# Performance work log

Measured on AMD Instinct MI355X. Metric: run time of the kernel, lower is better.

Reference implementation:

```python
import jax, jax.numpy as jnp
import numpy as np

B, N, M, C = 4, 2048, 576, 512
H, KVH, D = 8, 2, 64          # heads, kv heads, head_dim
E, TOPK, F = 8, 2, 2048       # experts, top-k, expert hidden (4*C)
EPS = 1e-6
NEG = -1e9


def setup_inputs() -> dict:
    key = jax.random.key(0)
    ks = iter(jax.random.split(key, 40))
    w = lambda shape, s=0.02: jax.random.normal(next(ks), shape, jnp.float32) * s
    d = {
        'x': jax.random.normal(next(ks), (B, N, C), jnp.float32),
        'vision_features': jax.random.normal(next(ks), (B, M, C), jnp.float32),
        'ln1_g': jnp.ones((C,), jnp.float32), 'ln1_b': jnp.zeros((C,), jnp.float32),
        'ln2_g': jnp.ones((C,), jnp.float32), 'ln2_b': jnp.zeros((C,), jnp.float32),
        'ln3_g': jnp.ones((C,), jnp.float32), 'ln3_b': jnp.zeros((C,), jnp.float32),
        # self-attention (GQA): q -> C, k/v -> KVH*D
        'sa_wq': w((C, C)), 'sa_bq': jnp.zeros((C,), jnp.float32),
        'sa_wk': w((C, KVH * D)), 'sa_bk': jnp.zeros((KVH * D,), jnp.float32),
        'sa_wv': w((C, KVH * D)), 'sa_bv': jnp.zeros((KVH * D,), jnp.float32),
        'sa_wo': w((C, C)), 'sa_bo': jnp.zeros((C,), jnp.float32),
        # cross-attention (GQA)
        'ca_wq': w((C, C)), 'ca_bq': jnp.zeros((C,), jnp.float32),
        'ca_wk': w((C, KVH * D)), 'ca_bk': jnp.zeros((KVH * D,), jnp.float32),
        'ca_wv': w((C, KVH * D)), 'ca_bv': jnp.zeros((KVH * D,), jnp.float32),
        'ca_wo': w((C, C)), 'ca_bo': jnp.zeros((C,), jnp.float32),
        # MoE: router + stacked expert MLPs (C -> F -> C, GELU)
        'router_w': w((C, E)), 'router_b': jnp.zeros((E,), jnp.float32),
        'e_w1': w((E, C, F)), 'e_b1': jnp.zeros((E, F), jnp.float32),
        'e_w2': w((E, F, C)), 'e_b2': jnp.zeros((E, C), jnp.float32),
    }
    return d


def _ln(x, g, b):
    mu = jnp.mean(x, -1, keepdims=True)
    var = jnp.mean(jnp.square(x - mu), -1, keepdims=True)
    return (x - mu) * jax.lax.rsqrt(var + EPS) * g + b


def _gqa_attn(xq, ctx, wq, bq, wk, bk, wv, bv, wo, bo, causal):
    b, n, c = xq.shape
    m = ctx.shape[1]
    q = (xq @ wq + bq).reshape(b, n, H, D).transpose(0, 2, 1, 3)      # bhnd
    k = (ctx @ wk + bk).reshape(b, m, KVH, D).transpose(0, 2, 1, 3)   # bgmd
    v = (ctx @ wv + bv).reshape(b, m, KVH, D).transpose(0, 2, 1, 3)
    rep = H // KVH
    k = jnp.repeat(k, rep, axis=1)  # repeat_interleave over head dim
    v = jnp.repeat(v, rep, axis=1)
    scores = jnp.einsum('bhnd,bhmd->bhnm', q, k) * (D ** -0.5)
    if causal:
        mask = jnp.tril(jnp.ones((n, m), bool))
        scores = jnp.where(mask, scores, NEG)
    a = jax.nn.softmax(scores, axis=-1)
    o = jnp.einsum('bhnm,bhmd->bhnd', a, v).transpose(0, 2, 1, 3).reshape(b, n, c)
    return o @ wo + bo


def _moe(x, router_w, router_b, e_w1, e_b1, e_w2, e_b2):
    logits = x @ router_w + router_b                    # [B,N,E]
    probs = jax.nn.softmax(logits, axis=-1)
    topv, topi = jax.lax.top_k(probs, TOPK)             # [B,N,K]
    topv = topv / jnp.sum(topv, -1, keepdims=True)      # renormalize top-k gates
    onehot = jax.nn.one_hot(topi, E, dtype=x.dtype)     # [B,N,K,E]
    gates = jnp.einsum('bnke,bnk->bne', onehot, topv)   # sparse gates, zeros off top-k
    h = jax.nn.gelu(jnp.einsum('bnc,ecf->bnef', x, e_w1) + e_b1)
    eo = jnp.einsum('bnef,efc->bnec', h, e_w2) + e_b2
    out = jnp.einsum('bne,bnec->bnc', gates, eo)
    # load-balance aux loss (Switch-style): E * sum_e f_e * P_e
    dispatch = jnp.sum(onehot, axis=2)                  # [B,N,E] routed mask
    f = jnp.mean(dispatch, axis=(0, 1))
    P = jnp.mean(probs, axis=(0, 1))
    aux = E * jnp.sum(f * P)
    return out, aux


def reference(x, vision_features,
              ln1_g, ln1_b, ln2_g, ln2_b, ln3_g, ln3_b,
              sa_wq, sa_bq, sa_wk, sa_bk, sa_wv, sa_bv, sa_wo, sa_bo,
              ca_wq, ca_bq, ca_wk, ca_bk, ca_wv, ca_bv, ca_wo, ca_bo,
              router_w, router_b, e_w1, e_b1, e_w2, e_b2):
    # pre-norm causal self-attn + residual
    h = _ln(x, ln1_g, ln1_b)
    x = x + _gqa_attn(h, h, sa_wq, sa_bq, sa_wk, sa_bk, sa_wv, sa_bv, sa_wo, sa_bo, True)
    # pre-norm cross-attn + residual
    h = _ln(x, ln2_g, ln2_b)
    x = x + _gqa_attn(h, vision_features, ca_wq, ca_bq, ca_wk, ca_bk, ca_wv, ca_bv, ca_wo, ca_bo, False)
    # pre-norm MoE FFN + residual
    h = _ln(x, ln3_g, ln3_b)
    m, aux = _moe(h, router_w, router_b, e_w1, e_b1, e_w2, e_b2)
    return x + m, aux
```

## Files before the change

kernel.cpp:

```cpp
#include <hip/hip_runtime.h>
#include <cstddef>
#include <cstdint>

#define B_   4
#define N_   2048
#define M_   576
#define C_   512
#define H_   8
#define KVH_ 2
#define D_   64
#define E_   8
#define F_   2048
#define BN_  (B_*N_)
#define BM_  (B_*M_)

typedef __attribute__((ext_vector_type(8))) short bf16x8;
typedef __attribute__((ext_vector_type(4))) float f32x4;

__device__ __forceinline__ unsigned short f2bf(float f) {
    union { float f; unsigned int u; } v; v.f = f;
    unsigned int r = v.u + 0x7FFFu + ((v.u >> 16) & 1u);
    return (unsigned short)(r >> 16);
}
__device__ __forceinline__ float bf2f(unsigned short u) {
    union { unsigned int u; float f; } v; v.u = ((unsigned int)u) << 16;
    return v.f;
}

typedef __attribute__((address_space(1))) void glb_void;
typedef __attribute__((address_space(3))) void lds_void;
__device__ __forceinline__ void gl2lds16(const unsigned short* g, unsigned short* l) {
    __builtin_amdgcn_global_load_lds((glb_void*)g, (lds_void*)l, 16, 0, 0);
}

__global__ __launch_bounds__(256) void prep_all(
    const float* __restrict__ sa_wq, const float* __restrict__ sa_wk,
    const float* __restrict__ sa_wv, const float* __restrict__ sa_wo,
    const float* __restrict__ ca_wq, const float* __restrict__ ca_wk,
    const float* __restrict__ ca_wv, const float* __restrict__ ca_wo,
    const float* __restrict__ e_w1, const float* __restrict__ e_w2,
    const float* __restrict__ vis,
    const float* __restrict__ sa_bk, const float* __restrict__ sa_bv,
    const float* __restrict__ ca_bk, const float* __restrict__ ca_bv,
    unsigned short* __restrict__ sa_wqt, unsigned short* __restrict__ sa_wkvt,
    unsigned short* __restrict__ sa_wot,
    unsigned short* __restrict__ ca_wqt, unsigned short* __restrict__ ca_wkvt,
    unsigned short* __restrict__ ca_wot,
    unsigned short* __restrict__ w1t, unsigned short* __restrict__ w2t,
    unsigned short* __restrict__ visbf,
    float* __restrict__ bkv_sa, float* __restrict__ bkv_ca,
    int* __restrict__ ctrl)
{
    __shared__ float T[32][33];
    int t = blockIdx.x;
    int tid = threadIdx.x;

    if (t < 17664) {
        const float* W; unsigned short* Wt; int K, N, kt, nt;
        if (t < 1280) {
            if (t < 256)      { W = sa_wq; Wt = sa_wqt; K = 512; N = 512; int r = t;        nt = r & 15; kt = r >> 4; }
            else if (t < 320) { W = sa_wk; Wt = sa_wkvt;            K = 512; N = 128; int r = t - 256; nt = r & 3;  kt = r >> 2; }
            else if (t < 384) { W = sa_wv; Wt = sa_wkvt + 128*512;  K = 512; N = 128; int r = t - 320; nt = r & 3;  kt = r >> 2; }
            else if (t < 640) { W = sa_wo; Wt = sa_wot; K = 512; N = 512; int r = t - 384;  nt = r & 15; kt = r >> 4; }
            else if (t < 896) { W = ca_wq; Wt = ca_wqt; K = 512; N = 512; int r = t - 640;  nt = r & 15; kt = r >> 4; }
            else if (t < 960) { W = ca_wk; Wt = ca_wkvt;            K = 512; N = 128; int r = t - 896; nt = r & 3;  kt = r >> 2; }
            else if (t < 1024){ W = ca_wv; Wt = ca_wkvt + 128*512;  K = 512; N = 128; int r = t - 960; nt = r & 3;  kt = r >> 2; }
            else              { W = ca_wo; Wt = ca_wot; K = 512; N = 512; int r = t - 1024; nt = r & 15; kt = r >> 4; }
        } else if (t < 9472) {
            int r = t - 1280; int e = r >> 10; r &= 1023;
            W = e_w1 + (size_t)e * C_ * F_; Wt = w1t + (size_t)e * C_ * F_;
            K = C_; N = F_; nt = r & 63; kt = r >> 6;
        } else {
            int r = t - 9472; int e = r >> 10; r &= 1023;
            W = e_w2 + (size_t)e * F_ * C_; Wt = w2t + (size_t)e * F_ * C_;
            K = F_; N = C_; nt = r & 15; kt = r >> 4;
        }
        int rr = tid >> 3, c4 = (tid & 7) * 4;
        int k0 = kt * 32, n0 = nt * 32;
        float4 v = *(const float4*)&W[(size_t)(k0 + rr) * N + n0 + c4];
        T[rr][c4 + 0] = v.x; T[rr][c4 + 1] = v.y; T[rr][c4 + 2] = v.z; T[rr][c4 + 3] = v.w;
        __syncthreads();
        ushort4 o;
        o.x = f2bf(T[c4 + 0][rr]); o.y = f2bf(T[c4 + 1][rr]);
        o.z = f2bf(T[c4 + 2][rr]); o.w = f2bf(T[c4 + 3][rr]);
        *(ushort4*)&Wt[(size_t)(n0 + rr) * K + k0 + c4] = o;
    } else if (t < 18816) {
        int i = (t - 17664) * 1024 + tid * 4;
        float4 v = *(const float4*)(vis + i);
        ushort4 o;
        o.x = f2bf(v.x); o.y = f2bf(v.y); o.z = f2bf(v.z); o.w = f2bf(v.w);
        *(ushort4*)(visbf + i) = o;
    } else {
        if (tid < 128) {
            bkv_sa[tid]       = sa_bk[tid];
            bkv_sa[128 + tid] = sa_bv[tid];
            bkv_ca[tid]       = ca_bk[tid];
            bkv_ca[128 + tid] = ca_bv[tid];
        }
        if (tid < 32) ctrl[tid] = 0;
    }
}

__global__ __launch_bounds__(256) void ln_bf(const float* __restrict__ x,
    const float* __restrict__ g, const float* __restrict__ b, unsigned short* __restrict__ out)
{
    int row = blockIdx.x;
    const float* xr = x + (size_t)row * C_;
    float s = 0.f, ss = 0.f;
    for (int c = threadIdx.x; c < C_; c += 256) { float v = xr[c]; s += v; ss += v * v; }
    __shared__ float S1[256], S2[256];
    S1[threadIdx.x] = s; S2[threadIdx.x] = ss;
    __syncthreads();
    for (int o = 128; o > 0; o >>= 1) {
        if (threadIdx.x < o) { S1[threadIdx.x] += S1[threadIdx.x + o]; S2[threadIdx.x] += S2[threadIdx.x + o]; }
        __syncthreads();
    }
    float mu  = S1[0] * (1.f / C_);
    float var = S2[0] * (1.f / C_) - mu * mu;
    float inv = rsqrtf(var + 1e-6f);
    unsigned short* orow = out + (size_t)row * C_;
    for (int c = threadIdx.x; c < C_; c += 256)
        orow[c] = f2bf((xr[c] - mu) * inv * g[c] + b[c]);
}

__global__ __launch_bounds__(256) void ln_dual(const float* __restrict__ x,
    const float* __restrict__ g, const float* __restrict__ b,
    float* __restrict__ outF, unsigned short* __restrict__ outBf)
{
    int row = blockIdx.x;
    const float* xr = x + (size_t)row * C_;
    float s = 0.f, ss = 0.f;
    for (int c = threadIdx.x; c < C_; c += 256) { float v = xr[c]; s += v; ss += v * v; }
    __shared__ float S1[256], S2[256];
    S1[threadIdx.x] = s; S2[threadIdx.x] = ss;
    __syncthreads();
    for (int o = 128; o > 0; o >>= 1) {
        if (threadIdx.x < o) { S1[threadIdx.x] += S1[threadIdx.x + o]; S2[threadIdx.x] += S2[threadIdx.x + o]; }
        __syncthreads();
    }
    float mu  = S1[0] * (1.f / C_);
    float var = S2[0] * (1.f / C_) - mu * mu;
    float inv = rsqrtf(var + 1e-6f);
    for (int c = threadIdx.x; c < C_; c += 256) {
        float v = (xr[c] - mu) * inv * g[c] + b[c];
        outF[(size_t)row * C_ + c] = v;
        outBf[(size_t)row * C_ + c] = f2bf(v);
    }
}

__global__ __launch_bounds__(256) void dense_mfma(
    const unsigned short* __restrict__ Abf,
    const unsigned short* __restrict__ Btbf,
    const float* __restrict__ bias,
    const float* __restrict__ xin,
    float* __restrict__ outF,
    unsigned short* __restrict__ outBf,
    unsigned short* __restrict__ outBf2,
    int N, int K, int mode, int NkPer)
{
    int row0 = blockIdx.y * 128;
    int col0 = blockIdx.x * 128;

    __shared__ unsigned short As[128 * 32];
    __shared__ unsigned short Bs[128 * 32];

    int tid = threadIdx.x;
    int lane = tid & 63, wid = tid >> 6;
    int lrow = lane >> 2;
    int cswz = (((lane & 3) ^ ((lane >> 3) & 3)) << 3);
    int ar0 = 16 * (wid * 2) + lrow;
    int ar1 = ar0 + 16;
    const unsigned short* gA0 = Abf + (size_t)(row0 + ar0) * K + cswz;
    const unsigned short* gA1 = Abf + (size_t)(row0 + ar1) * K + cswz;
    const unsigned short* gB0 = Btbf + (size_t)(col0 + ar0) * K + cswz;
    const unsigned short* gB1 = Btbf + (size_t)(col0 + ar1) * K + cswz;
    unsigned short* lA0 = As + (wid * 2) * 512;
    unsigned short* lA1 = lA0 + 512;
    unsigned short* lB0 = Bs + (wid * 2) * 512;
    unsigned short* lB1 = lB0 + 512;

    int wm0 = (wid & 1) * 64, wn0 = (wid >> 1) * 64;
    int lm = lane & 15, lq = lane >> 4;
    int swb = (lq ^ ((lm >> 1) & 3)) << 3;
    int aoff[4], boff[4];
#pragma unroll
    for (int i = 0; i < 4; i++) {
        aoff[i] = (wm0 + 16 * i + lm) * 32 + swb;
        boff[i] = (wn0 + 16 * i + lm) * 32 + swb;
    }

    f32x4 acc[4][4];
#pragma unroll
    for (int i = 0; i < 4; i++)
#pragma unroll
        for (int j = 0; j < 4; j++)
            acc[i][j] = (f32x4){0.f, 0.f, 0.f, 0.f};

    for (int k0 = 0; k0 < K; k0 += 32) {
        __syncthreads();
        gl2lds16(gA0 + k0, lA0);
        gl2lds16(gA1 + k0, lA1);
        gl2lds16(gB0 + k0, lB0);
        gl2lds16(gB1 + k0, lB1);
        __syncthreads();

        bf16x8 av[4], bv[4];
#pragma unroll
        for (int i = 0; i < 4; i++) av[i] = *(const bf16x8*)&As[aoff[i]];
#pragma unroll
        for (int i = 0; i < 4; i++) bv[i] = *(const bf16x8*)&Bs[boff[i]];
#pragma unroll
        for (int mi = 0; mi < 4; mi++)
#pragma unroll
            for (int ni = 0; ni < 4; ni++)
                acc[mi][ni] = __builtin_amdgcn_mfma_f32_16x16x32_bf16(av[mi], bv[ni], acc[mi][ni], 0, 0, 0);
    }

#pragma unroll
    for (int mi = 0; mi < 4; mi++) {
#pragma unroll
        for (int ri = 0; ri < 4; ri++) {
            int gr = row0 + wm0 + 16 * mi + lq * 4 + ri;
            if (mode == 3) {
#pragma unroll
                for (int ni = 0; ni < 4; ni++) {
                    int gc = col0 + wn0 + 16 * ni + lm;
                    float v = acc[mi][ni][ri] + bias[gc];
                    if (gc < 128) {
                        outBf[(size_t)gr * 128 + gc] = f2bf(v);
                    } else {
                        int bb = gr / NkPer;
                        int mm = gr - bb * NkPer;
                        outBf2[((size_t)bb * 128 + (gc - 128)) * NkPer + mm] = f2bf(v);
                    }
                }
            } else if (mode == 1) {
                size_t orow = (size_t)gr * N;
#pragma unroll
                for (int ni = 0; ni < 4; ni++) {
                    int gc = col0 + wn0 + 16 * ni + lm;
                    outF[orow + gc] += acc[mi][ni][ri] + bias[gc];
                }
            } else if (mode == 4) {
                size_t orow = (size_t)gr * N;
#pragma unroll
                for (int ni = 0; ni < 4; ni++) {
                    int gc = col0 + wn0 + 16 * ni + lm;
                    outF[orow + gc] = xin[orow + gc] + acc[mi][ni][ri] + bias[gc];
                }
            } else {
                size_t orow = (size_t)gr * N;
#pragma unroll
                for (int ni = 0; ni < 4; ni++) {
                    int gc = col0 + wn0 + 16 * ni + lm;
                    outBf[orow + gc] = f2bf(acc[mi][ni][ri] + bias[gc]);
                }
            }
        }
    }
}

__global__ __launch_bounds__(256) void attn_mfma(
    const unsigned short* __restrict__ Q,
    const unsigned short* __restrict__ K,
    const unsigned short* __restrict__ Vt,
    unsigned short* __restrict__ Obf,
    float* __restrict__ Opart,
    float* __restrict__ Lpart,
    int NkPer, int causal)
{
    __shared__ unsigned short Qs[64 * 72];
    __shared__ unsigned short Ks[64 * 72];
    __shared__ unsigned short Vs[64 * 72];
    unsigned short* Ps = Qs;

    int tid = threadIdx.x;
    int qt = blockIdx.x, bh = blockIdx.y, z = blockIdx.z;
    int b = bh >> 3, h = bh & 7, g = h >> 2;
    int q0 = qt * 64;

#pragma unroll
    for (int i = 0; i < 2; i++) {
        int s = tid + (i << 8);
        int r = s >> 3, c8 = (s & 7) << 3;
        *(uint4*)&Qs[r * 72 + c8] =
            *(const uint4*)&Q[(size_t)(b * N_ + q0 + r) * C_ + h * D_ + c8];
    }
    __syncthreads();

    int lane = tid & 63, wid = tid >> 6;
    int lm = lane & 15, lq = lane >> 4;
    int arow = wid * 16 + lm;

    bf16x8 qf[2];
    qf[0] = *(const bf16x8*)&Qs[arow * 72 + lq * 8];
    qf[1] = *(const bf16x8*)&Qs[arow * 72 + lq * 8 + 32];

    float lsum[4];
    f32x4 of[4];
#pragma unroll
    for (int i = 0; i < 4; i++) { lsum[i] = 0.f; of[i] = (f32x4){0.f,0.f,0.f,0.f}; }

    int nkt = causal ? (qt + 1) : ((NkPer + 63) >> 6);
    int nz = gridDim.z;
    int per = (nkt + nz - 1) / nz;
    int kt0 = z * per;
    int kt1 = min(nkt, kt0 + per);

    for (int kt = kt0; kt < kt1; kt++) {
        int k0 = kt << 6;
        __syncthreads();
#pragma unroll
        for (int i = 0; i < 2; i++) {
            int s = tid + (i << 8);
            int r = s >> 3, c8 = (s & 7) << 3;
            *(uint4*)&Ks[r * 72 + c8] =
                *(const uint4*)&K[(size_t)(b * NkPer + k0 + r) * (KVH_ * D_) + g * D_ + c8];
            *(uint4*)&Vs[r * 72 + c8] =
                *(const uint4*)&Vt[(size_t)(b * (KVH_ * D_) + g * D_ + r) * NkPer + k0 + c8];
        }
        __syncthreads();

        f32x4 sf[4];
#pragma unroll
        for (int i = 0; i < 4; i++) sf[i] = (f32x4){0.f,0.f,0.f,0.f};
#pragma unroll
        for (int ks = 0; ks < 2; ks++) {
#pragma unroll
            for (int ni = 0; ni < 4; ni++) {
                bf16x8 bv = *(const bf16x8*)&Ks[(16 * ni + lm) * 72 + lq * 8 + 32 * ks];
                sf[ni] = __builtin_amdgcn_mfma_f32_16x16x32_bf16(qf[ks], bv, sf[ni], 0, 0, 0);
            }
        }

        bool diag = causal && (k0 + 63 > q0 + wid * 16);
#pragma unroll
        for (int ni = 0; ni < 4; ni++)
#pragma unroll
            for (int ri = 0; ri < 4; ri++) {
                float v = sf[ni][ri] * 0.125f - 8.f;
                if (diag && (k0 + 16 * ni + lm > q0 + wid * 16 + lq * 4 + ri)) v = -1e30f;
                float p = __expf(v);
                sf[ni][ri] = p;
                lsum[ri] += p;
            }

#pragma unroll
        for (int ni = 0; ni < 4; ni++)
#pragma unroll
            for (int ri = 0; ri < 4; ri++)
                Ps[(wid * 16 + lq * 4 + ri) * 72 + 16 * ni + lm] = f2bf(sf[ni][ri]);
        __syncthreads();

        bf16x8 pf0 = *(const bf16x8*)&Ps[arow * 72 + lq * 8];
        bf16x8 pf1 = *(const bf16x8*)&Ps[arow * 72 + lq * 8 + 32];
#pragma unroll
        for (int ni = 0; ni < 4; ni++) {
            bf16x8 vv0 = *(const bf16x8*)&Vs[(16 * ni + lm) * 72 + lq * 8];
            bf16x8 vv1 = *(const bf16x8*)&Vs[(16 * ni + lm) * 72 + lq * 8 + 32];
            of[ni] = __builtin_amdgcn_mfma_f32_16x16x32_bf16(pf0, vv0, of[ni], 0, 0, 0);
            of[ni] = __builtin_amdgcn_mfma_f32_16x16x32_bf16(pf1, vv1, of[ni], 0, 0, 0);
        }
    }

#pragma unroll
    for (int ri = 0; ri < 4; ri++) {
        float s = lsum[ri];
        s += __shfl_xor(s, 1);
        s += __shfl_xor(s, 2);
        s += __shfl_xor(s, 4);
        s += __shfl_xor(s, 8);
        lsum[ri] = s;
    }

    if (nz == 1) {
#pragma unroll
        for (int ri = 0; ri < 4; ri++) {
            float inv = 1.f / lsum[ri];
            int q = q0 + wid * 16 + lq * 4 + ri;
            size_t orow = (size_t)(b * N_ + q) * C_ + h * D_;
#pragma unroll
            for (int ni = 0; ni < 4; ni++)
                Obf[orow + 16 * ni + lm] = f2bf(of[ni][ri] * inv);
        }
    } else {
        size_t zofs = (size_t)z * BN_ * C_;
#pragma unroll
        for (int ri = 0; ri < 4; ri++) {
            int q = q0 + wid * 16 + lq * 4 + ri;
            size_t orow = zofs + (size_t)(b * N_ + q) * C_ + h * D_;
#pragma unroll
            for (int ni = 0; ni < 4; ni++)
                Opart[orow + 16 * ni + lm] = of[ni][ri];
            if (lm == 0)
                Lpart[(size_t)z * (B_ * H_ * N_) + bh * N_ + q] = lsum[ri];
        }
    }
}

__global__ __launch_bounds__(256) void attn_combine(const float* __restrict__ Opart,
    const float* __restrict__ Lpart, unsigned short* __restrict__ Obf)
{
    int flat = (blockIdx.x * 256 + threadIdx.x) * 4;
    int row = flat >> 9, col = flat & 511;
    int b = row >> 11, q = row & (N_ - 1), h = col >> 6;
    int bh = b * 8 + h;
    float l = Lpart[bh * N_ + q] + Lpart[B_ * H_ * N_ + bh * N_ + q];
    float inv = 1.f / l;
    float4 o0 = *(const float4*)&Opart[flat];
    float4 o1 = *(const float4*)&Opart[(size_t)BN_ * C_ + flat];
    ushort4 o;
    o.x = f2bf((o0.x + o1.x) * inv); o.y = f2bf((o0.y + o1.y) * inv);
    o.z = f2bf((o0.z + o1.z) * inv); o.w = f2bf((o0.w + o1.w) * inv);
    *(ushort4*)&Obf[flat] = o;
}

__global__ __launch_bounds__(256) void router_logits(const float* __restrict__ X,
    const float* __restrict__ RW, const float* __restrict__ RB,
    float* __restrict__ gprobs, int* __restrict__ topi, float* __restrict__ gatesv)
{
    int lane = threadIdx.x & 63;
    int t = blockIdx.x * 4 + (threadIdx.x >> 6);
    const float* xr = X + (size_t)t * C_;
    float p[8] = {};
    for (int i = 0; i < 8; i++) {
        int c = i * 64 + lane;
        float xv = xr[c];
#pragma unroll
        for (int e = 0; e < 8; e++) p[e] = fmaf(xv, RW[c * 8 + e], p[e]);
    }
#pragma unroll
    for (int e = 0; e < 8; e++) {
        float v = p[e];
        v += __shfl_xor(v, 32, 64);
        v += __shfl_xor(v, 16, 64);
        v += __shfl_xor(v, 8, 64);
        v += __shfl_xor(v, 4, 64);
        v += __shfl_xor(v, 2, 64);
        v += __shfl_xor(v, 1, 64);
        p[e] = v;
    }
    if (lane == 0) {
        float logits[8], mx = -1e30f;
        for (int e = 0; e < 8; e++) { logits[e] = p[e] + RB[e]; mx = fmaxf(mx, logits[e]); }
        float pr[8], sum = 0.f;
        for (int e = 0; e < 8; e++) { pr[e] = expf(logits[e] - mx); sum += pr[e]; }
        float inv = 1.f / sum;
        for (int e = 0; e < 8; e++) { pr[e] *= inv; gprobs[t * 8 + e] = pr[e]; }
        int i1 = 0;
        for (int e = 1; e < 8; e++) if (pr[e] > pr[i1]) i1 = e;
        int i2 = (i1 == 0) ? 1 : 0;
        for (int e = 0; e < 8; e++) if (e != i1 && pr[e] > pr[i2]) i2 = e;
        float v1 = pr[i1], v2 = pr[i2], sg = 1.f / (v1 + v2);
        topi[t * 2]     = i1;  topi[t * 2 + 1]   = i2;
        gatesv[t * 2]   = v1 * sg;  gatesv[t * 2 + 1] = v2 * sg;
    }
}

__global__ __launch_bounds__(256) void router_reduce(const float* __restrict__ gprobs,
    const int* __restrict__ topi, int* __restrict__ ctrl, float* __restrict__ psum)
{
    __shared__ float fs[256];
    __shared__ int   is_[256];
    int bid = blockIdx.x, tid = threadIdx.x;
    if (bid < 8) {
        float s = 0.f;
        for (int t = tid; t < BN_; t += 256) s += gprobs[t * 8 + bid];
        fs[tid] = s; __syncthreads();
        for (int o = 128; o > 0; o >>= 1) { if (tid < o) fs[tid] += fs[tid + o]; __syncthreads(); }
        if (tid == 0) psum[bid] = fs[0];
    } else {
        int e = bid - 8, c = 0;
        for (int i = tid; i < BN_ * 2; i += 256) c += (topi[i] == e);
        is_[tid] = c; __syncthreads();
        for (int o = 128; o > 0; o >>= 1) { if (tid < o) is_[tid] += is_[tid + o]; __syncthreads(); }
        if (tid == 0) ctrl[e] = is_[0];
    }
}

__global__ void router_offsets(int* __restrict__ ctrl)
{
    if (threadIdx.x == 0 && blockIdx.x == 0) {
        int off = 0;
        for (int e = 0; e < 8; e++) {
            ctrl[16 + e] = off;
            off += (ctrl[e] + 127) & ~127;
        }
        ctrl[24] = off;
    }
}

__global__ __launch_bounds__(256) void router_scatter(const int* __restrict__ topi,
    const float* __restrict__ gatesv, int* __restrict__ rowtok,
    int* __restrict__ slotidx, int* __restrict__ ctrl)
{
    __shared__ int lcnt[8];
    __shared__ int lbase[8];
    int tid = threadIdx.x;
    int t = blockIdx.x * 256 + tid;
    if (tid < 8) lcnt[tid] = 0;
    __syncthreads();
    int e0 = topi[t * 2], e1 = topi[t * 2 + 1];
    int p0 = atomicAdd(&lcnt[e0], 1);
    int p1 = atomicAdd(&lcnt[e1], 1);
    __syncthreads();
    if (tid < 8) lbase[tid] = atomicAdd(&ctrl[8 + tid], lcnt[tid]);
    __syncthreads();
    int s0 = ctrl[16 + e0] + lbase[e0] + p0;
    int s1 = ctrl[16 + e1] + lbase[e1] + p1;
    rowtok[s0] = t;
    rowtok[s1] = t;
    slotidx[t * 2]     = s0;
    slotidx[t * 2 + 1] = s1;
}

__global__ __launch_bounds__(256) void moe_mfma(
    const unsigned short* __restrict__ Abf,
    const unsigned short* __restrict__ Btbf,
    const float* __restrict__ biasAll,
    unsigned short* __restrict__ outBf,
    const int* __restrict__ rowtok,
    const int* __restrict__ ctrl,
    int N, int K, int mode)
{
    int e = blockIdx.z;
    int cnt = ctrl[e];
    int row0 = blockIdx.x * 128;
    if (row0 >= cnt) return;
    int off = ctrl[16 + e];
    int col0 = blockIdx.y * 128;
    const unsigned short* Bt = Btbf + (size_t)e * N * K;
    const float* bias = biasAll + (size_t)e * N;

    __shared__ unsigned short As[128 * 32];
    __shared__ unsigned short Bs[128 * 32];
    __shared__ __align__(16) unsigned short Cs[4][32 * 72];
    __shared__ int toks[128];

    int tid = threadIdx.x;
    if (mode == 1 && tid < 128) {
        int gl = row0 + tid;
        toks[tid] = rowtok[off + (gl < cnt ? gl : 0)];
    }
    __syncthreads();

    int lane = tid & 63, wid = tid >> 6;
    int lrow = lane >> 2;
    int cswz = (((lane & 3) ^ ((lane >> 3) & 3)) << 3);
    int ar0 = 16 * (wid * 2) + lrow;
    int ar1 = ar0 + 16;
    const unsigned short *gA0, *gA1;
    if (mode == 1) {
        gA0 = Abf + (size_t)toks[ar0] * K + cswz;
        gA1 = Abf + (size_t)toks[ar1] * K + cswz;
    } else {
        gA0 = Abf + (size_t)(off + row0 + ar0) * K + cswz;
        gA1 = Abf + (size_t)(off + row0 + ar1) * K + cswz;
    }
    const unsigned short* gB0 = Bt + (size_t)(col0 + ar0) * K + cswz;
    const unsigned short* gB1 = Bt + (size_t)(col0 + ar1) * K + cswz;
    unsigned short* lA0 = As + (wid * 2) * 512;
    unsigned short* lA1 = lA0 + 512;
    unsigned short* lB0 = Bs + (wid * 2) * 512;
    unsigned short* lB1 = lB0 + 512;

    int wm0 = (wid & 1) * 64, wn0 = (wid >> 1) * 64;
    int lm = lane & 15, lq = lane >> 4;
    int swb = (lq ^ ((lm >> 1) & 3)) << 3;
    int aoff[4], boff[4];
#pragma unroll
    for (int i = 0; i < 4; i++) {
        aoff[i] = (wm0 + 16 * i + lm) * 32 + swb;
        boff[i] = (wn0 + 16 * i + lm) * 32 + swb;
    }

    f32x4 acc[4][4];
#pragma unroll
    for (int i = 0; i < 4; i++)
#pragma unroll
        for (int j = 0; j < 4; j++)
            acc[i][j] = (f32x4){0.f, 0.f, 0.f, 0.f};

    for (int k0 = 0; k0 < K; k0 += 32) {
        __syncthreads();
        gl2lds16(gA0 + k0, lA0);
        gl2lds16(gA1 + k0, lA1);
        gl2lds16(gB0 + k0, lB0);
        gl2lds16(gB1 + k0, lB1);
        __syncthreads();

        bf16x8 av[4], bv[4];
#pragma unroll
        for (int i = 0; i < 4; i++) av[i] = *(const bf16x8*)&As[aoff[i]];
#pragma unroll
        for (int i = 0; i < 4; i++) bv[i] = *(const bf16x8*)&Bs[boff[i]];
#pragma unroll
        for (int mi = 0; mi < 4; mi++)
#pragma unroll
            for (int ni = 0; ni < 4; ni++)
                acc[mi][ni] = __builtin_amdgcn_mfma_f32_16x16x32_bf16(av[mi], bv[ni], acc[mi][ni], 0, 0, 0);
    }

    unsigned short* cs = Cs[wid];
#pragma unroll
    for (int p = 0; p < 2; p++) {
#pragma unroll
        for (int m2 = 0; m2 < 2; m2++) {
            int mi = 2 * p + m2;
#pragma unroll
            for (int ri = 0; ri < 4; ri++) {
                int gl = row0 + wm0 + 16 * mi + lq * 4 + ri;
                bool valid = gl < cnt;
#pragma unroll
                for (int ni = 0; ni < 4; ni++) {
                    int gc = col0 + wn0 + 16 * ni + lm;
                    float xv = acc[mi][ni][ri] + bias[gc];
                    float hv;
                    if (mode == 1) {
                        float z = 0.7978845608f * xv * fmaf(0.044715f, xv * xv, 1.f);
                        hv = valid ? __fdividef(xv, 1.f + __expf(-2.f * z)) : 0.f;
                    } else {
                        hv = xv;
                    }
                    cs[(m2 * 16 + lq * 4 + ri) * 72 + 16 * ni + lm] = f2bf(hv);
                }
            }
        }
        int rr = lane >> 1;
        int ch = (lane & 1) * 32;
        int gl2 = row0 + wm0 + 32 * p + rr;
        size_t orow = (size_t)(off + gl2) * N + col0 + wn0 + ch;
        const unsigned short* rsrc = &cs[rr * 72 + ch];
#pragma unroll
        for (int j = 0; j < 4; j++)
            *(uint4*)&outBf[orow + j * 8] = *(const uint4*)&rsrc[j * 8];
    }
}

__global__ __launch_bounds__(256) void moe_combine(const unsigned short* __restrict__ slots,
    const int* __restrict__ slotidx, const float* __restrict__ gatesv,
    float* __restrict__ out)
{
    int flat = (blockIdx.x * 256 + threadIdx.x) * 4;
    int t = flat >> 9, c = flat & 511;
    int s0 = slotidx[t * 2], s1 = slotidx[t * 2 + 1];
    float g0 = gatesv[t * 2], g1 = gatesv[t * 2 + 1];
    ushort4 a = *(const ushort4*)&slots[(size_t)s0 * C_ + c];
    ushort4 b = *(const ushort4*)&slots[(size_t)s1 * C_ + c];
    float4 o = *(float4*)&out[flat];
    o.x += g0 * bf2f(a.x) + g1 * bf2f(b.x);
    o.y += g0 * bf2f(a.y) + g1 * bf2f(b.y);
    o.z += g0 * bf2f(a.z) + g1 * bf2f(b.z);
    o.w += g0 * bf2f(a.w) + g1 * bf2f(b.w);
    *(float4*)&out[flat] = o;
}

__global__ void aux_kernel(const int* __restrict__ ctrl, const float* __restrict__ psum,
                           float* __restrict__ outaux)
{
    if (threadIdx.x == 0 && blockIdx.x == 0) {
        float s = 0.f;
        for (int e = 0; e < 8; e++)
            s += ((float)ctrl[e] / (float)BN_) * (psum[e] / (float)BN_);
        outaux[0] = 8.f * s;
    }
}

extern "C" void kernel_launch(void* const* d_in, const int* in_sizes, int n_in,
                              void* d_out, int out_size, void* d_ws, size_t ws_size,
                              hipStream_t stream)
{
    const float* x      = (const float*)d_in[0];
    const float* vis    = (const float*)d_in[1];
    const float* ln1g   = (const float*)d_in[2];
    const float* ln1b   = (const float*)d_in[3];
    const float* ln2g   = (const float*)d_in[4];
    const float* ln2b   = (const float*)d_in[5];
    const float* ln3g   = (const float*)d_in[6];
    const float* ln3b   = (const float*)d_in[7];
    const float* sa_wq  = (const float*)d_in[8];
    const float* sa_bq  = (const float*)d_in[9];
    const float* sa_wk  = (const float*)d_in[10];
    const float* sa_bk  = (const float*)d_in[11];
    const float* sa_wv  = (const float*)d_in[12];
    const float* sa_bv  = (const float*)d_in[13];
    const float* sa_wo  = (const float*)d_in[14];
    const float* sa_bo  = (const float*)d_in[15];
    const float* ca_wq  = (const float*)d_in[16];
    const float* ca_bq  = (const float*)d_in[17];
    const float* ca_wk  = (const float*)d_in[18];
    const float* ca_bk  = (const float*)d_in[19];
    const float* ca_wv  = (const float*)d_in[20];
    const float* ca_bv  = (const float*)d_in[21];
    const float* ca_wo  = (const float*)d_in[22];
    const float* ca_bo  = (const float*)d_in[23];
    const float* rw     = (const float*)d_in[24];
    const float* rb     = (const float*)d_in[25];
    const float* e_w1   = (const float*)d_in[26];
    const float* e_b1   = (const float*)d_in[27];
    const float* e_w2   = (const float*)d_in[28];
    const float* e_b2   = (const float*)d_in[29];

    float* out = (float*)d_out;

    char* ws = (char*)d_ws;
    size_t off = 0;
    auto alloc = [&](size_t bytes) -> void* {
        void* p = ws + off;
        off = (off + bytes + 255) & ~(size_t)255;
        return p;
    };
    float* hbuf    = (float*)alloc((size_t)BN_ * C_ * 4);
    unsigned short* hbz = (unsigned short*)alloc((size_t)BN_ * C_ * 2);
    unsigned short* visbf = (unsigned short*)alloc((size_t)BM_ * C_ * 2);
    unsigned short* eoslots = (unsigned short*)hbuf;
    char* ureg = (char*)alloc((size_t)17408 * F_ * 2);
    unsigned short* moeH = (unsigned short*)ureg;
    unsigned short* qbf  = (unsigned short*)(ureg);
    unsigned short* obf  = (unsigned short*)(ureg + (size_t)BN_ * C_ * 2);
    unsigned short* kbf  = (unsigned short*)(ureg + (size_t)BN_ * C_ * 4);
    unsigned short* vtbf = (unsigned short*)(ureg + (size_t)BN_ * C_ * 4 + (size_t)BN_ * KVH_ * D_ * 2);
    float* opart = (float*)(ureg + (size_t)BN_ * C_ * 4 + (size_t)BN_ * KVH_ * D_ * 4);
    float* lpart = (float*)(ureg + (size_t)BN_ * C_ * 4 + (size_t)BN_ * KVH_ * D_ * 4
                                 + (size_t)2 * BN_ * C_ * 4);
    unsigned short* sa_wqt = (unsigned short*)alloc((size_t)C_ * C_ * 2);
    unsigned short* sa_wkvt = (unsigned short*)alloc((size_t)C_ * 2 * KVH_ * D_ * 2);
    unsigned short* sa_wot = (unsigned short*)alloc((size_t)C_ * C_ * 2);
    unsigned short* ca_wqt = (unsigned short*)alloc((size_t)C_ * C_ * 2);
    unsigned short* ca_wkvt = (unsigned short*)alloc((size_t)C_ * 2 * KVH_ * D_ * 2);
    unsigned short* ca_wot = (unsigned short*)alloc((size_t)C_ * C_ * 2);
    float* bkv_sa = (float*)alloc(256 * 4);
    float* bkv_ca = (float*)alloc(256 * 4);
    unsigned short* w1t  = (unsigned short*)alloc((size_t)E_ * C_ * F_ * 2);
    unsigned short* w2t  = (unsigned short*)alloc((size_t)E_ * F_ * C_ * 2);
    float* gprobs  = (float*)alloc((size_t)BN_ * 8 * 4);
    int*   topi    = (int*)  alloc((size_t)BN_ * 2 * 4);
    float* gatesv  = (float*)alloc((size_t)BN_ * 2 * 4);
    int*   rowtok  = (int*)  alloc(17408 * 4);
    int*   slotidx = (int*)  alloc((size_t)BN_ * 2 * 4);
    int*   ctrl    = (int*)  alloc(256);
    float* psum    = (float*)((char*)ctrl + 128);
    (void)ws_size; (void)in_sizes; (void)n_in; (void)out_size;

    prep_all<<<18817, 256, 0, stream>>>(
        sa_wq, sa_wk, sa_wv, sa_wo, ca_wq, ca_wk, ca_wv, ca_wo,
        e_w1, e_w2, vis, sa_bk, sa_bv, ca_bk, ca_bv,
        sa_wqt, sa_wkvt, sa_wot, ca_wqt, ca_wkvt, ca_wot,
        w1t, w2t, visbf, bkv_sa, bkv_ca, ctrl);

    ln_bf<<<BN_, 256, 0, stream>>>(x, ln1g, ln1b, hbz);
    dense_mfma<<<dim3(4, 64), 256, 0, stream>>>(hbz, sa_wqt, sa_bq, nullptr, nullptr, qbf, nullptr, C_, C_, 0, 0);
    dense_mfma<<<dim3(2, 64), 256, 0, stream>>>(hbz, sa_wkvt, bkv_sa, nullptr, nullptr, kbf, vtbf, 256, C_, 3, N_);
    attn_mfma<<<dim3(N_/64, B_*H_, 2), 256, 0, stream>>>(qbf, kbf, vtbf, nullptr, opart, lpart, N_, 1);
    attn_combine<<<(BN_*C_)/1024, 256, 0, stream>>>(opart, lpart, obf);
    dense_mfma<<<dim3(4, 64), 256, 0, stream>>>(obf, sa_wot, sa_bo, x, out, nullptr, nullptr, C_, C_, 4, 0);

    ln_bf<<<BN_, 256, 0, stream>>>(out, ln2g, ln2b, hbz);
    dense_mfma<<<dim3(4, 64), 256, 0, stream>>>(hbz, ca_wqt, ca_bq, nullptr, nullptr, qbf, nullptr, C_, C_, 0, 0);
    dense_mfma<<<dim3(2, 18), 256, 0, stream>>>(visbf, ca_wkvt, bkv_ca, nullptr, nullptr, kbf, vtbf, 256, C_, 3, M_);
    attn_mfma<<<dim3(N_/64, B_*H_, 1), 256, 0, stream>>>(qbf, kbf, vtbf, obf, nullptr, nullptr, M_, 0);
    dense_mfma<<<dim3(4, 64), 256, 0, stream>>>(obf, ca_wot, ca_bo, nullptr, out, nullptr, nullptr, C_, C_, 1, 0);

    ln_dual<<<BN_, 256, 0, stream>>>(out, ln3g, ln3b, hbuf, hbz);
    router_logits<<<BN_/4, 256, 0, stream>>>(hbuf, rw, rb, gprobs, topi, gatesv);
    router_reduce<<<16, 256, 0, stream>>>(gprobs, topi, ctrl, psum);
    router_offsets<<<1, 1, 0, stream>>>(ctrl);
    router_scatter<<<BN_/256, 256, 0, stream>>>(topi, gatesv, rowtok, slotidx, ctrl);
    moe_mfma<<<dim3(BN_/128, F_/128, E_), 256, 0, stream>>>(
        hbz, w1t, e_b1, moeH, rowtok, ctrl, F_, C_, 1);
    moe_mfma<<<dim3(BN_/128, C_/128, E_), 256, 0, stream>>>(
        moeH, w2t, e_b2, eoslots, rowtok, ctrl, C_, F_, 2);
    moe_combine<<<(BN_*C_)/1024, 256, 0, stream>>>(eoslots, slotidx, gatesv, out);
    aux_kernel<<<1, 1, 0, stream>>>(ctrl, psum, out + (size_t)BN_ * C_);
}
```

Baseline: 729.7 us.

## Deepen MoE GEMM K-tile to 64 with XOR swizzle and direct epilogue stores

The MoE expert GEMM kernel now stages 64-wide K slices per iteration with an 8-way XOR swizzle, halving the number of barrier pairs per tile. The grid is transposed so column tiles vary fastest, letting consecutive blocks share the same A rows in cache. The LDS-staged coalesced epilogue is replaced by direct scalar bf16 stores from accumulators, which frees LDS but produces narrower, less coalesced global writes.

```diff
diff --git a/kernel.cpp b/kernel.cpp
--- a/kernel.cpp
+++ b/kernel.cpp
@@ -525,16 +525,15 @@
 {
     int e = blockIdx.z;
     int cnt = ctrl[e];
-    int row0 = blockIdx.x * 128;
+    int row0 = blockIdx.y * 128;
     if (row0 >= cnt) return;
     int off = ctrl[16 + e];
-    int col0 = blockIdx.y * 128;
+    int col0 = blockIdx.x * 128;
     const unsigned short* Bt = Btbf + (size_t)e * N * K;
     const float* bias = biasAll + (size_t)e * N;
 
-    __shared__ unsigned short As[128 * 32];
-    __shared__ unsigned short Bs[128 * 32];
-    __shared__ __align__(16) unsigned short Cs[4][32 * 72];
+    __shared__ unsigned short As[128 * 64];
+    __shared__ unsigned short Bs[128 * 64];
     __shared__ int toks[128];
 
     int tid = threadIdx.x;
@@ -545,33 +544,33 @@
     __syncthreads();
 
     int lane = tid & 63, wid = tid >> 6;
-    int lrow = lane >> 2;
-    int cswz = (((lane & 3) ^ ((lane >> 3) & 3)) << 3);
-    int ar0 = 16 * (wid * 2) + lrow;
-    int ar1 = ar0 + 16;
-    const unsigned short *gA0, *gA1;
-    if (mode == 1) {
-        gA0 = Abf + (size_t)toks[ar0] * K + cswz;
-        gA1 = Abf + (size_t)toks[ar1] * K + cswz;
-    } else {
-        gA0 = Abf + (size_t)(off + row0 + ar0) * K + cswz;
-        gA1 = Abf + (size_t)(off + row0 + ar1) * K + cswz;
-    }
-    const unsigned short* gB0 = Bt + (size_t)(col0 + ar0) * K + cswz;
-    const unsigned short* gB1 = Bt + (size_t)(col0 + ar1) * K + cswz;
-    unsigned short* lA0 = As + (wid * 2) * 512;
-    unsigned short* lA1 = lA0 + 512;
-    unsigned short* lB0 = Bs + (wid * 2) * 512;
-    unsigned short* lB1 = lB0 + 512;
+    int r8 = lane >> 3;
+    size_t asrc[4], bsrc[4];
+    unsigned short *adst[4], *bdst[4];
+#pragma unroll
+    for (int i = 0; i < 4; i++) {
+        int rA = wid * 32 + i * 8 + r8;
+        int srcc = (((lane & 7) ^ (rA & 7)) << 3);
+        size_t arow = (mode == 1) ? (size_t)toks[rA] * K
+                                  : (size_t)(off + row0 + rA) * K;
+        asrc[i] = arow + srcc;
+        bsrc[i] = (size_t)(col0 + rA) * K + srcc;
+        adst[i] = As + (wid * 32 + i * 8) * 64;
+        bdst[i] = Bs + (wid * 32 + i * 8) * 64;
+    }
 
     int wm0 = (wid & 1) * 64, wn0 = (wid >> 1) * 64;
     int lm = lane & 15, lq = lane >> 4;
-    int swb = (lq ^ ((lm >> 1) & 3)) << 3;
-    int aoff[4], boff[4];
+    int x7 = lm & 7;
+    int aoff[4][2], boff[4][2];
 #pragma unroll
     for (int i = 0; i < 4; i++) {
-        aoff[i] = (wm0 + 16 * i + lm) * 32 + swb;
-        boff[i] = (wn0 + 16 * i + lm) * 32 + swb;
+#pragma unroll
+        for (int ks = 0; ks < 2; ks++) {
+            int swz = (((ks << 2) + lq) ^ x7) << 3;
+            aoff[i][ks] = (wm0 + 16 * i + lm) * 64 + swz;
+            boff[i][ks] = (wn0 + 16 * i + lm) * 64 + swz;
+        }
     }
 
     f32x4 acc[4][4];
@@ -581,59 +580,56 @@
         for (int j = 0; j < 4; j++)
             acc[i][j] = (f32x4){0.f, 0.f, 0.f, 0.f};
 
-    for (int k0 = 0; k0 < K; k0 += 32) {
-        __syncthreads();
-        gl2lds16(gA0 + k0, lA0);
-        gl2lds16(gA1 + k0, lA1);
-        gl2lds16(gB0 + k0, lB0);
-        gl2lds16(gB1 + k0, lB1);
-        __syncthreads();
-
-        bf16x8 av[4], bv[4];
-#pragma unroll
-        for (int i = 0; i < 4; i++) av[i] = *(const bf16x8*)&As[aoff[i]];
-#pragma unroll
-        for (int i = 0; i < 4; i++) bv[i] = *(const bf16x8*)&Bs[boff[i]];
-#pragma unroll
-        for (int mi = 0; mi < 4; mi++)
-#pragma unroll
-            for (int ni = 0; ni < 4; ni++)
-                acc[mi][ni] = __builtin_amdgcn_mfma_f32_16x16x32_bf16(av[mi], bv[ni], acc[mi][ni], 0, 0, 0);
-    }
-
-    unsigned short* cs = Cs[wid];
-#pragma unroll
-    for (int p = 0; p < 2; p++) {
-#pragma unroll
-        for (int m2 = 0; m2 < 2; m2++) {
-            int mi = 2 * p + m2;
-#pragma unroll
-            for (int ri = 0; ri < 4; ri++) {
-                int gl = row0 + wm0 + 16 * mi + lq * 4 + ri;
-                bool valid = gl < cnt;
+    for (int k0 = 0; k0 < K; k0 += 64) {
+        __syncthreads();
+#pragma unroll
+        for (int i = 0; i < 4; i++) {
+            gl2lds16(Abf + asrc[i] + k0, adst[i]);
+            gl2lds16(Bt  + bsrc[i] + k0, bdst[i]);
+        }
+        __syncthreads();
+
+#pragma unroll
+        for (int ks = 0; ks < 2; ks++) {
+            bf16x8 av[4], bv[4];
+#pragma unroll
+            for (int i = 0; i < 4; i++) av[i] = *(const bf16x8*)&As[aoff[i][ks]];
+#pragma unroll
+            for (int i = 0; i < 4; i++) bv[i] = *(const bf16x8*)&Bs[boff[i][ks]];
+#pragma unroll
+            for (int mi = 0; mi < 4; mi++)
+#pragma unroll
+                for (int ni = 0; ni < 4; ni++)
+                    acc[mi][ni] = __builtin_amdgcn_mfma_f32_16x16x32_bf16(av[mi], bv[ni], acc[mi][ni], 0, 0, 0);
+        }
+    }
+
+#pragma unroll
+    for (int mi = 0; mi < 4; mi++) {
+#pragma unroll
+        for (int ri = 0; ri < 4; ri++) {
+            int gl = row0 + wm0 + 16 * mi + lq * 4 + ri;
+            size_t orow = (size_t)(off + gl) * N;
+            if (mode == 1) {
 #pragma unroll
                 for (int ni = 0; ni < 4; ni++) {
                     int gc = col0 + wn0 + 16 * ni + lm;
-                    float xv = acc[mi][ni][ri] + bias[gc];
-                    float hv;
-                    if (mode == 1) {
+                    float hv = 0.f;
+                    if (gl < cnt) {
+                        float xv = acc[mi][ni][ri] + bias[gc];
                         float z = 0.7978845608f * xv * fmaf(0.044715f, xv * xv, 1.f);
-                        hv = valid ? __fdividef(xv, 1.f + __expf(-2.f * z)) : 0.f;
-                    } else {
-                        hv = xv;
+                        hv = __fdividef(xv, 1.f + __expf(-2.f * z));
                     }
-                    cs[(m2 * 16 + lq * 4 + ri) * 72 + 16 * ni + lm] = f2bf(hv);
+                    outBf[orow + gc] = f2bf(hv);
+                }
+            } else {
+#pragma unroll
+                for (int ni = 0; ni < 4; ni++) {
+                    int gc = col0 + wn0 + 16 * ni + lm;
+                    outBf[orow + gc] = f2bf(acc[mi][ni][ri] + bias[gc]);
                 }
             }
         }
-        int rr = lane >> 1;
-        int ch = (lane & 1) * 32;
-        int gl2 = row0 + wm0 + 32 * p + rr;
-        size_t orow = (size_t)(off + gl2) * N + col0 + wn0 + ch;
-        const unsigned short* rsrc = &cs[rr * 72 + ch];
-#pragma unroll
-        for (int j = 0; j < 4; j++)
-            *(uint4*)&outBf[orow + j * 8] = *(const uint4*)&rsrc[j * 8];
     }
 }
 
@@ -766,9 +762,9 @@
     router_reduce<<<16, 256, 0, stream>>>(gprobs, topi, ctrl, psum);
     router_offsets<<<1, 1, 0, stream>>>(ctrl);
     router_scatter<<<BN_/256, 256, 0, stream>>>(topi, gatesv, rowtok, slotidx, ctrl);
-    moe_mfma<<<dim3(BN_/128, F_/128, E_), 256, 0, stream>>>(
+    moe_mfma<<<dim3(F_/128, BN_/128, E_), 256, 0, stream>>>(
         hbz, w1t, e_b1, moeH, rowtok, ctrl, F_, C_, 1);
-    moe_mfma<<<dim3(BN_/128, C_/128, E_), 256, 0, stream>>>(
+    moe_mfma<<<dim3(C_/128, BN_/128, E_), 256, 0, stream>>>(
         moeH, w2t, e_b2, eoslots, rowtok, ctrl, C_, F_, 2);
     moe_combine<<<(BN_*C_)/1024, 256, 0, stream>>>(eoslots, slotidx, gatesv, out);
     aux_kernel<<<1, 1, 0, stream>>>(ctrl, psum, out + (size_t)BN_ * C_);
```

Result: faster. 660.1 us (-9.5%).
